# Optimization experiments

Measured on AMD Instinct MI355X. Metric: run time of the kernel, lower is better.

## Reference

```python
import jax, jax.numpy as jnp
import numpy as np

N_HEAD = 16
N_EMBD = 1024

def setup_inputs() -> dict:
    key = jax.random.key(0)
    ks = jax.random.split(key, 5)
    C = N_EMBD
    x = jax.random.normal(ks[0], (4, 2048, C), dtype=jnp.float32)
    s = 1.0 / np.sqrt(C)
    W_attn = jax.random.normal(ks[1], (C, 3 * C), dtype=jnp.float32) * s
    b_attn = jax.random.normal(ks[2], (3 * C,), dtype=jnp.float32) * 0.02
    W_proj = jax.random.normal(ks[3], (C, C), dtype=jnp.float32) * s
    b_proj = jax.random.normal(ks[4], (C,), dtype=jnp.float32) * 0.02
    return {"x": x, "W_attn": W_attn, "b_attn": b_attn, "W_proj": W_proj, "b_proj": b_proj}

def reference(x, W_attn, b_attn, W_proj, b_proj):
    B, T, C = x.shape
    H = C // N_HEAD
    qkv = x @ W_attn + b_attn  # [B,T,3C]
    q, k, v = jnp.split(qkv, 3, axis=2)
    # [B,T,C] -> [B,nh,T,H]
    q = q.reshape(B, T, N_HEAD, H).transpose(0, 2, 1, 3)
    k = k.reshape(B, T, N_HEAD, H).transpose(0, 2, 1, 3)
    v = v.reshape(B, T, N_HEAD, H).transpose(0, 2, 1, 3)
    att = jnp.einsum('bhqd,bhkd->bhqk', q, k) * (1.0 / np.sqrt(H).astype(np.float32))
    causal = jnp.tril(jnp.ones((T, T), dtype=bool))  # [T,T]
    att = jnp.where(causal, att, -jnp.inf)
    att = jax.nn.softmax(att, axis=-1)
    y = jnp.einsum('bhqk,bhkd->bhqd', att, v)
    y = y.transpose(0, 2, 1, 3).reshape(B, T, C)
    return y @ W_proj + b_proj
```

## Files before the change

### kernel.cpp

```cpp
#include <hip/hip_runtime.h>
#include <math.h>

#define T_LEN 2048
#define C_DIM 1024
#define C3    3072
#define NHEAD 16
#define HDIM  64

typedef __attribute__((ext_vector_type(8))) __bf16 bf16x8;
typedef __attribute__((ext_vector_type(8))) unsigned short u16x8;
typedef __attribute__((ext_vector_type(4))) float f32x4;
typedef unsigned short ushort_t;

#define QK_SCALE 0.180336878f

#if defined(__has_builtin)
#if __has_builtin(__builtin_amdgcn_exp2f)
#define FAST_EXP2(x) __builtin_amdgcn_exp2f(x)
#endif
#endif
#ifndef FAST_EXP2
#define FAST_EXP2(x) exp2f(x)
#endif

__device__ __forceinline__ ushort_t f2bf(float f) {
    unsigned int u = __float_as_uint(f);
    unsigned int r = (u + 0x7FFFu + ((u >> 16) & 1u)) >> 16;
    return (ushort_t)r;
}

#define GLL16(g, l) __builtin_amdgcn_global_load_lds( \
    (const __attribute__((address_space(1))) void*)(g), \
    (__attribute__((address_space(3))) void*)(l), 16, 0, 0)

__global__ __launch_bounds__(256) void prep_inputs(
    const float* __restrict__ x, ushort_t* __restrict__ xb,
    const float* __restrict__ W1, ushort_t* __restrict__ Wt1,
    const float* __restrict__ W2, ushort_t* __restrict__ Wt2)
{
    __shared__ float t[64][65];
    const int bx = blockIdx.x;
    if (bx < 8192) {
        const int i = bx * 256 + threadIdx.x;
        const float4 v = ((const float4*)x)[i];
        ushort4 o;
        o.x = f2bf(v.x); o.y = f2bf(v.y); o.z = f2bf(v.z); o.w = f2bf(v.w);
        ((ushort4*)xb)[i] = o;
        return;
    }
    const float* W; ushort_t* Wt; int N, n0, k0;
    if (bx < 8960) {
        const int tt = bx - 8192;
        W = W1; Wt = Wt1; N = C3;
        n0 = (tt % 48) * 64; k0 = (tt / 48) * 64;
    } else {
        const int tt = bx - 8960;
        W = W2; Wt = Wt2; N = C_DIM;
        n0 = (tt % 16) * 64; k0 = (tt / 16) * 64;
    }
    const int K = C_DIM;
    const int c = threadIdx.x & 63, r4 = threadIdx.x >> 6;
#pragma unroll
    for (int i = 0; i < 16; i++) {
        int r = i * 4 + r4;
        t[r][c] = W[(size_t)(k0 + r) * N + n0 + c];
    }
    __syncthreads();
#pragma unroll
    for (int i = 0; i < 16; i++) {
        int r = i * 4 + r4;
        Wt[(size_t)(n0 + r) * K + k0 + c] = f2bf(t[c][r]);
    }
}

template <bool OUT_BF16, bool QSCALE>
__global__ __launch_bounds__(256, 3) void gemm_bt_mfma(
    const ushort_t* __restrict__ A, const ushort_t* __restrict__ Bt,
    const float* __restrict__ bias, void* __restrict__ Cv,
    int M, int N, int K)
{
    __shared__ ushort_t Alds[128 * 64];
    __shared__ ushort_t Blds[128 * 64];

    const int tid = threadIdx.x;
    const int m0 = blockIdx.y * 128;
    const int n0 = blockIdx.x * 128;
    const int w = tid >> 6;
    const int ln = tid & 63;
    const int quad = ln >> 4;
    const int r16 = ln & 15;
    const int wr0 = (w & 1) * 64;
    const int wc0 = (w >> 1) * 64;

    f32x4 acc[4][4] = {};

    const int srow = tid >> 3;
    const int csrc8 = ((tid & 7) ^ (srow & 7)) * 8;
    const int sw = r16 & 7;

    for (int k0 = 0; k0 < K; k0 += 64) {
#pragma unroll
        for (int rr = 0; rr < 4; rr++) {
            const ushort_t* ga = A + (size_t)(m0 + rr * 32 + srow) * K + k0 + csrc8;
            GLL16(ga, Alds + rr * 2048 + tid * 8);
            const ushort_t* gb = Bt + (size_t)(n0 + rr * 32 + srow) * K + k0 + csrc8;
            GLL16(gb, Blds + rr * 2048 + tid * 8);
        }
        __syncthreads();

#pragma unroll
        for (int s = 0; s < 2; s++) {
            const int cpos = ((4 * s + quad) ^ sw) * 8;
            bf16x8 af[4], bfr[4];
#pragma unroll
            for (int i = 0; i < 4; i++)
                af[i] = *(const bf16x8*)(Alds + (wr0 + i * 16 + r16) * 64 + cpos);
#pragma unroll
            for (int j = 0; j < 4; j++)
                bfr[j] = *(const bf16x8*)(Blds + (wc0 + j * 16 + r16) * 64 + cpos);
#pragma unroll
            for (int i = 0; i < 4; i++)
#pragma unroll
                for (int j = 0; j < 4; j++)
                    acc[i][j] = __builtin_amdgcn_mfma_f32_16x16x32_bf16(
                        af[i], bfr[j], acc[i][j], 0, 0, 0);
        }
        __syncthreads();
    }

    const float scl = (QSCALE && n0 < C_DIM) ? QK_SCALE : 1.0f;

#pragma unroll
    for (int j = 0; j < 4; j++) {
        const int col = n0 + wc0 + j * 16 + r16;
        const float bv = bias[col];
#pragma unroll
        for (int i = 0; i < 4; i++) {
            const int rowb = m0 + wr0 + i * 16 + quad * 4;
#pragma unroll
            for (int r = 0; r < 4; r++) {
                const float v = (acc[i][j][r] + bv) * scl;
                if (OUT_BF16)
                    ((ushort_t*)Cv)[(size_t)(rowb + r) * N + col] = f2bf(v);
                else
                    ((float*)Cv)[(size_t)(rowb + r) * N + col] = v;
            }
        }
    }
}

__global__ __launch_bounds__(256) void transpose_v(
    const ushort_t* __restrict__ qkv, ushort_t* __restrict__ vtg)
{
    __shared__ ushort_t Ts[64][72];
    const int t0 = blockIdx.x * 64;
    const int bh = blockIdx.y;
    const int b = bh >> 4, h = bh & 15;
    const ushort_t* src = qkv + (size_t)b * T_LEN * C3 + 2 * C_DIM + h * HDIM;
    const int tid = threadIdx.x;
    {
        const int r = tid >> 2, cs = (tid & 3) * 16;
        *(u16x8*)(&Ts[r][cs])     = *(const u16x8*)(src + (size_t)(t0 + r) * C3 + cs);
        *(u16x8*)(&Ts[r][cs + 8]) = *(const u16x8*)(src + (size_t)(t0 + r) * C3 + cs + 8);
    }
    __syncthreads();
    {
        const int d = tid >> 2, ts0 = (tid & 3) * 16;
        ushort_t* dst = vtg + ((size_t)bh * HDIM + d) * T_LEN + t0 + ts0;
        u16x8 o0, o1;
#pragma unroll
        for (int j = 0; j < 8; j++) o0[j] = Ts[ts0 + j][d];
#pragma unroll
        for (int j = 0; j < 8; j++) o1[j] = Ts[ts0 + 8 + j][d];
        *(u16x8*)dst = o0;
        *(u16x8*)(dst + 8) = o1;
    }
}

#define QPITCH 72

__device__ __forceinline__ void softmax_store(
    f32x4 (&s)[4], float& lacc, ushort_t* __restrict__ QP,
    int prow, int quad)
{
#pragma unroll
    for (int mb = 0; mb < 4; mb++) {
        const float p0 = FAST_EXP2(s[mb][0]);
        const float p1 = FAST_EXP2(s[mb][1]);
        const float p2 = FAST_EXP2(s[mb][2]);
        const float p3 = FAST_EXP2(s[mb][3]);
        lacc += (p0 + p1) + (p2 + p3);
        uint2 pk;
        pk.x = __builtin_amdgcn_perm(__float_as_uint(p1), __float_as_uint(p0), 0x07060302u);
        pk.y = __builtin_amdgcn_perm(__float_as_uint(p3), __float_as_uint(p2), 0x07060302u);
        *(uint2*)(QP + prow * QPITCH + mb * 16 + quad * 4) = pk;
    }
}

__device__ __forceinline__ void mask_diag(f32x4 (&s)[4], int qloc, int quad)
{
#pragma unroll
    for (int mb = 0; mb < 4; mb++)
#pragma unroll
        for (int r = 0; r < 4; r++)
            if (mb * 16 + quad * 4 + r > qloc) s[mb][r] = -1e30f;
}

__global__ __launch_bounds__(256) void attn_flash_mfma5(
    const ushort_t* __restrict__ qkv, const ushort_t* __restrict__ vtg,
    ushort_t* __restrict__ y)
{
    __shared__ ushort_t QP[128 * QPITCH];
    __shared__ ushort_t Ks[64 * 64];
    __shared__ ushort_t Vs[64 * 64];

    const int i = blockIdx.x;
    const int bh = blockIdx.y;
    const int b = bh >> 4, h = bh & 15;
    const int qA0 = i * 64;
    const int qB0 = (31 - i) * 64;
    const int lastkt = 31 - i;

    const int tid = threadIdx.x;
    const int w = tid >> 6;
    const int ln = tid & 63;
    const int quad = ln >> 4;
    const int r16 = ln & 15;
    const int qloc = w * 16 + r16;
    const int prowA = qloc;
    const int prowB = 64 + qloc;

    const int srow = tid >> 3;
    const int csrc8 = ((tid & 7) ^ (srow & 7)) * 8;
    const int cpos0 = ((quad ^ (r16 & 7))) * 8;

    const ushort_t* baseq = qkv + (size_t)b * T_LEN * C3 + h * HDIM;
    const ushort_t* basek = baseq + C_DIM;
    const ushort_t* vrow = vtg + (size_t)bh * HDIM * T_LEN;

#pragma unroll
    for (int it = 0; it < 4; it++) {
        int e = tid + it * 256;
        int r = e >> 3, c8 = (e & 7) * 8;
        int gq = (r < 64) ? (qA0 + r) : (qB0 + r - 64);
        *(u16x8*)(QP + r * QPITCH + c8) =
            *(const u16x8*)(baseq + (size_t)gq * C3 + c8);
    }
    __syncthreads();

    bf16x8 aqA[2], aqB[2];
#pragma unroll
    for (int s = 0; s < 2; s++) {
        aqA[s] = *(const bf16x8*)(QP + prowA * QPITCH + s * 32 + quad * 8);
        aqB[s] = *(const bf16x8*)(QP + prowB * QPITCH + s * 32 + quad * 8);
    }

    f32x4 oA[4] = {}, oB[4] = {};
    float lA = 0.0f, lB = 0.0f;

    for (int kt = 0; kt <= lastkt; kt++) {
        const int k0 = kt * 64;
        __syncthreads();

#pragma unroll
        for (int rr = 0; rr < 2; rr++) {
            const ushort_t* gk = basek + (size_t)(k0 + rr * 32 + srow) * C3 + csrc8;
            GLL16(gk, Ks + rr * 2048 + tid * 8);
            const ushort_t* gv = vrow + (size_t)(rr * 32 + srow) * T_LEN + k0 + csrc8;
            GLL16(gv, Vs + rr * 2048 + tid * 8);
        }
        __syncthreads();

        if (kt <= i) {
            f32x4 sA[4] = {}, sB[4] = {};
#pragma unroll
            for (int s = 0; s < 2; s++)
#pragma unroll
                for (int mb = 0; mb < 4; mb++) {
                    const bf16x8 ak = *(const bf16x8*)(Ks + (mb * 16 + r16) * 64 + (cpos0 ^ (s * 32)));
                    sA[mb] = __builtin_amdgcn_mfma_f32_16x16x32_bf16(ak, aqA[s], sA[mb], 0, 0, 0);
                    sB[mb] = __builtin_amdgcn_mfma_f32_16x16x32_bf16(ak, aqB[s], sB[mb], 0, 0, 0);
                }
            if (kt == i) mask_diag(sA, qloc, quad);
            softmax_store(sA, lA, QP, prowA, quad);
            softmax_store(sB, lB, QP, prowB, quad);
#pragma unroll
            for (int s = 0; s < 2; s++) {
                const bf16x8 bpA = *(const bf16x8*)(QP + prowA * QPITCH + s * 32 + quad * 8);
                const bf16x8 bpB = *(const bf16x8*)(QP + prowB * QPITCH + s * 32 + quad * 8);
#pragma unroll
                for (int mb = 0; mb < 4; mb++) {
                    const bf16x8 av = *(const bf16x8*)(Vs + (mb * 16 + r16) * 64 + (cpos0 ^ (s * 32)));
                    oA[mb] = __builtin_amdgcn_mfma_f32_16x16x32_bf16(av, bpA, oA[mb], 0, 0, 0);
                    oB[mb] = __builtin_amdgcn_mfma_f32_16x16x32_bf16(av, bpB, oB[mb], 0, 0, 0);
                }
            }
        } else {
            f32x4 sB[4] = {};
#pragma unroll
            for (int s = 0; s < 2; s++)
#pragma unroll
                for (int mb = 0; mb < 4; mb++) {
                    const bf16x8 ak = *(const bf16x8*)(Ks + (mb * 16 + r16) * 64 + (cpos0 ^ (s * 32)));
                    sB[mb] = __builtin_amdgcn_mfma_f32_16x16x32_bf16(ak, aqB[s], sB[mb], 0, 0, 0);
                }
            if (kt == lastkt) mask_diag(sB, qloc, quad);
            softmax_store(sB, lB, QP, prowB, quad);
#pragma unroll
            for (int s = 0; s < 2; s++) {
                const bf16x8 bpB = *(const bf16x8*)(QP + prowB * QPITCH + s * 32 + quad * 8);
#pragma unroll
                for (int mb = 0; mb < 4; mb++) {
                    const bf16x8 av = *(const bf16x8*)(Vs + (mb * 16 + r16) * 64 + (cpos0 ^ (s * 32)));
                    oB[mb] = __builtin_amdgcn_mfma_f32_16x16x32_bf16(av, bpB, oB[mb], 0, 0, 0);
                }
            }
        }
    }

    lA += __shfl_xor(lA, 16); lA += __shfl_xor(lA, 32);
    lB += __shfl_xor(lB, 16); lB += __shfl_xor(lB, 32);
    {
        const float invA = 1.0f / lA;
        ushort_t* yp = y + ((size_t)(b * T_LEN + qA0 + qloc)) * C_DIM + h * HDIM;
#pragma unroll
        for (int mb = 0; mb < 4; mb++) {
            ushort4 o;
            o.x = f2bf(oA[mb][0] * invA);
            o.y = f2bf(oA[mb][1] * invA);
            o.z = f2bf(oA[mb][2] * invA);
            o.w = f2bf(oA[mb][3] * invA);
            *(ushort4*)(yp + mb * 16 + quad * 4) = o;
        }
    }
    {
        const float invB = 1.0f / lB;
        ushort_t* yp = y + ((size_t)(b * T_LEN + qB0 + qloc)) * C_DIM + h * HDIM;
#pragma unroll
        for (int mb = 0; mb < 4; mb++) {
            ushort4 o;
            o.x = f2bf(oB[mb][0] * invB);
            o.y = f2bf(oB[mb][1] * invB);
            o.z = f2bf(oB[mb][2] * invB);
            o.w = f2bf(oB[mb][3] * invB);
            *(ushort4*)(yp + mb * 16 + quad * 4) = o;
        }
    }
}

extern "C" void kernel_launch(void* const* d_in, const int* in_sizes, int n_in,
                              void* d_out, int out_size, void* d_ws, size_t ws_size,
                              hipStream_t stream)
{
    const float* x      = (const float*)d_in[0];
    const float* W_attn = (const float*)d_in[1];
    const float* b_attn = (const float*)d_in[2];
    const float* W_proj = (const float*)d_in[3];
    const float* b_proj = (const float*)d_in[4];
    float* out = (float*)d_out;

    const int M = 4 * T_LEN;
    char* ws = (char*)d_ws;
    ushort_t* qkv = (ushort_t*)ws;
    ushort_t* xb  = (ushort_t*)(ws + 50331648);
    ushort_t* Wt1 = (ushort_t*)(ws + 67108864);
    ushort_t* yb  = (ushort_t*)(ws + 73400320);
    ushort_t* Wt2 = (ushort_t*)(ws + 90177536);
    ushort_t* vtg = (ushort_t*)(ws + 92274688);

    prep_inputs<<<9216, 256, 0, stream>>>(x, xb, W_attn, Wt1, W_proj, Wt2);

    gemm_bt_mfma<true, true><<<dim3(C3 / 128, M / 128), 256, 0, stream>>>(
        xb, Wt1, b_attn, qkv, M, C3, C_DIM);

    transpose_v<<<dim3(T_LEN / 64, 4 * NHEAD), 256, 0, stream>>>(qkv, vtg);

    attn_flash_mfma5<<<dim3(16, 4 * NHEAD), 256, 0, stream>>>(qkv, vtg, yb);

    gemm_bt_mfma<false, false><<<dim3(C_DIM / 128, M / 128), 256, 0, stream>>>(
        yb, Wt2, b_proj, out, M, C_DIM, C_DIM);
}
```

Before: 276.2 us.

## Double-buffer K/V tiles in flash attention to overlap loads with MFMA

K and V shared-memory tiles are doubled so the next key tile is fetched while the current one is being computed on. The first tile is prefetched before the Q load. The loop now needs only one barrier per iteration instead of a load-then-barrier sequence. This hides global-to-LDS latency and removes a sync, at the cost of extra LDS per block, which may reduce occupancy.

```diff
diff --git a/kernel.cpp b/kernel.cpp
--- a/kernel.cpp
+++ b/kernel.cpp
@@ -206,13 +206,25 @@
             if (mb * 16 + quad * 4 + r > qloc) s[mb][r] = -1e30f;
 }
 
+#define STAGE_KV(kt_, buf_) do {                                              \
+    const int _k0 = (kt_) * 64;                                               \
+    const int _bo = (buf_) * 4096;                                            \
+    _Pragma("unroll")                                                         \
+    for (int rr = 0; rr < 2; rr++) {                                          \
+        const ushort_t* gk = basek + (size_t)(_k0 + rr * 32 + srow) * C3 + csrc8; \
+        GLL16(gk, Ks + _bo + rr * 2048 + tid * 8);                            \
+        const ushort_t* gv = vrow + (size_t)(rr * 32 + srow) * T_LEN + _k0 + csrc8; \
+        GLL16(gv, Vs + _bo + rr * 2048 + tid * 8);                            \
+    }                                                                         \
+} while (0)
+
 __global__ __launch_bounds__(256) void attn_flash_mfma5(
     const ushort_t* __restrict__ qkv, const ushort_t* __restrict__ vtg,
     ushort_t* __restrict__ y)
 {
     __shared__ ushort_t QP[128 * QPITCH];
-    __shared__ ushort_t Ks[64 * 64];
-    __shared__ ushort_t Vs[64 * 64];
+    __shared__ ushort_t Ks[2 * 64 * 64];
+    __shared__ ushort_t Vs[2 * 64 * 64];
 
     const int i = blockIdx.x;
     const int bh = blockIdx.y;
@@ -238,6 +250,8 @@
     const ushort_t* basek = baseq + C_DIM;
     const ushort_t* vrow = vtg + (size_t)bh * HDIM * T_LEN;
 
+    STAGE_KV(0, 0);
+
 #pragma unroll
     for (int it = 0; it < 4; it++) {
         int e = tid + it * 256;
@@ -259,17 +273,11 @@
     float lA = 0.0f, lB = 0.0f;
 
     for (int kt = 0; kt <= lastkt; kt++) {
-        const int k0 = kt * 64;
         __syncthreads();
 
-#pragma unroll
-        for (int rr = 0; rr < 2; rr++) {
-            const ushort_t* gk = basek + (size_t)(k0 + rr * 32 + srow) * C3 + csrc8;
-            GLL16(gk, Ks + rr * 2048 + tid * 8);
-            const ushort_t* gv = vrow + (size_t)(rr * 32 + srow) * T_LEN + k0 + csrc8;
-            GLL16(gv, Vs + rr * 2048 + tid * 8);
-        }
-        __syncthreads();
+        if (kt < lastkt) STAGE_KV(kt + 1, (kt + 1) & 1);
+
+        const int kb = (kt & 1) * 4096;
 
         if (kt <= i) {
             f32x4 sA[4] = {}, sB[4] = {};
@@ -277,7 +285,7 @@
             for (int s = 0; s < 2; s++)
 #pragma unroll
                 for (int mb = 0; mb < 4; mb++) {
-                    const bf16x8 ak = *(const bf16x8*)(Ks + (mb * 16 + r16) * 64 + (cpos0 ^ (s * 32)));
+                    const bf16x8 ak = *(const bf16x8*)(Ks + kb + (mb * 16 + r16) * 64 + (cpos0 ^ (s * 32)));
                     sA[mb] = __builtin_amdgcn_mfma_f32_16x16x32_bf16(ak, aqA[s], sA[mb], 0, 0, 0);
                     sB[mb] = __builtin_amdgcn_mfma_f32_16x16x32_bf16(ak, aqB[s], sB[mb], 0, 0, 0);
                 }
@@ -290,7 +298,7 @@
                 const bf16x8 bpB = *(const bf16x8*)(QP + prowB * QPITCH + s * 32 + quad * 8);
 #pragma unroll
                 for (int mb = 0; mb < 4; mb++) {
-                    const bf16x8 av = *(const bf16x8*)(Vs + (mb * 16 + r16) * 64 + (cpos0 ^ (s * 32)));
+                    const bf16x8 av = *(const bf16x8*)(Vs + kb + (mb * 16 + r16) * 64 + (cpos0 ^ (s * 32)));
                     oA[mb] = __builtin_amdgcn_mfma_f32_16x16x32_bf16(av, bpA, oA[mb], 0, 0, 0);
                     oB[mb] = __builtin_amdgcn_mfma_f32_16x16x32_bf16(av, bpB, oB[mb], 0, 0, 0);
                 }
@@ -301,7 +309,7 @@
             for (int s = 0; s < 2; s++)
 #pragma unroll
                 for (int mb = 0; mb < 4; mb++) {
-                    const bf16x8 ak = *(const bf16x8*)(Ks + (mb * 16 + r16) * 64 + (cpos0 ^ (s * 32)));
+                    const bf16x8 ak = *(const bf16x8*)(Ks + kb + (mb * 16 + r16) * 64 + (cpos0 ^ (s * 32)));
                     sB[mb] = __builtin_amdgcn_mfma_f32_16x16x32_bf16(ak, aqB[s], sB[mb], 0, 0, 0);
                 }
             if (kt == lastkt) mask_diag(sB, qloc, quad);
@@ -311,7 +319,7 @@
                 const bf16x8 bpB = *(const bf16x8*)(QP + prowB * QPITCH + s * 32 + quad * 8);
 #pragma unroll
                 for (int mb = 0; mb < 4; mb++) {
-                    const bf16x8 av = *(const bf16x8*)(Vs + (mb * 16 + r16) * 64 + (cpos0 ^ (s * 32)));
+                    const bf16x8 av = *(const bf16x8*)(Vs + kb + (mb * 16 + r16) * 64 + (cpos0 ^ (s * 32)));
                     oB[mb] = __builtin_amdgcn_mfma_f32_16x16x32_bf16(av, bpB, oB[mb], 0, 0, 0);
                 }
             }
```

Measured after the change: 280.3 us. No clear change (+1.5%).
